# Optimization experiments

Measured on AMD Instinct MI355X. Metric: run time of the kernel, lower is better.

The kernel has to match this reference:

```python
import jax, jax.numpy as jnp
import numpy as np

E, H, B, S = 512, 8, 8, 1024  # embed_dim, n_head, batch, n_agent (sequence)
DH = E // H
DECAY_SCALING = 1.0


def _rmsnorm(x, scale, eps=1e-6):
    return x * jax.lax.rsqrt(jnp.mean(x * x, axis=-1, keepdims=True) + eps) * scale


def _groupnorm(y, scale, bias, n_head, eps=1e-5):
    # GroupNorm with num_groups = n_head over the feature axis (flax semantics).
    b, s, e = y.shape
    yg = y.reshape(b, s, n_head, e // n_head)
    mu = jnp.mean(yg, axis=-1, keepdims=True)
    var = jnp.var(yg, axis=-1, keepdims=True)
    yn = (yg - mu) * jax.lax.rsqrt(var + eps)
    return yn.reshape(b, s, e) * scale + bias


def _decay_kappas(n_head, scaling):
    # RetNet multi-scale decays: 1 - exp(linspace(log(1/32), log(1/512), H))
    k = 1.0 - jnp.exp(jnp.linspace(jnp.log(1.0 / 32.0), jnp.log(1.0 / 512.0), n_head))
    return (k * scaling).astype(jnp.float32)


def _msr(key_x, query_x, value_x, wq, wk, wv, wg, wo, gs, gb, kappas):
    # Parallel multi-scale retention (masked / causal, full_self_retention=False).
    b, s, e = query_x.shape
    h = wq.shape[0]
    q = jnp.einsum('bse,hed->bhsd', query_x, wq)
    k = jnp.einsum('bse,hed->bhsd', key_x, wk)
    v = jnp.einsum('bse,hed->bhsd', value_x, wv)
    n = jnp.arange(s)
    diff = n[:, None] - n[None, :]
    causal = diff >= 0
    expnt = jnp.where(causal, diff, 0).astype(q.dtype)
    # D[h,n,m] = kappa_h^(n-m) for n>=m else 0
    D = jnp.where(causal[None], kappas[:, None, None] ** expnt[None], 0.0)
    scores = jnp.einsum('bhnd,bhmd->bhnm', q, k) * D[None]  # [B,H,S,S]
    ret = jnp.einsum('bhnm,bhmd->bhnd', scores, v)
    ret = ret.transpose(0, 2, 1, 3).reshape(b, s, e)
    ret = _groupnorm(ret, gs, gb, h)
    return (jax.nn.swish(query_x @ wg) * ret) @ wo


def _swiglu(x, w_gate, w_lin, w_out):
    return (jax.nn.swish(x @ w_gate) * (x @ w_lin)) @ w_out


def setup_inputs() -> dict:
    key = jax.random.key(0)
    ks = jax.random.split(key, 20)
    sc = 0.02
    d = {
        'x': jax.random.normal(ks[0], (B, S, E), jnp.float32),
        'obs_rep': jax.random.normal(ks[1], (B, S, E), jnp.float32),
        # retention 1 params
        'wq1': jax.random.normal(ks[2], (H, E, DH), jnp.float32) * sc,
        'wk1': jax.random.normal(ks[3], (H, E, DH), jnp.float32) * sc,
        'wv1': jax.random.normal(ks[4], (H, E, DH), jnp.float32) * sc,
        'wg1': jax.random.normal(ks[5], (E, E), jnp.float32) * sc,
        'wo1': jax.random.normal(ks[6], (E, E), jnp.float32) * sc,
        'gs1': jnp.ones((E,), jnp.float32),
        'gb1': jnp.zeros((E,), jnp.float32),
        # retention 2 params
        'wq2': jax.random.normal(ks[7], (H, E, DH), jnp.float32) * sc,
        'wk2': jax.random.normal(ks[8], (H, E, DH), jnp.float32) * sc,
        'wv2': jax.random.normal(ks[9], (H, E, DH), jnp.float32) * sc,
        'wg2': jax.random.normal(ks[10], (E, E), jnp.float32) * sc,
        'wo2': jax.random.normal(ks[11], (E, E), jnp.float32) * sc,
        'gs2': jnp.ones((E,), jnp.float32),
        'gb2': jnp.zeros((E,), jnp.float32),
        # RMSNorm scales
        'ln1_s': jnp.ones((E,), jnp.float32),
        'ln2_s': jnp.ones((E,), jnp.float32),
        'ln3_s': jnp.ones((E,), jnp.float32),
        # SwiGLU(hidden=E, input=E)
        'ffn_w_lin': jax.random.normal(ks[12], (E, E), jnp.float32) * sc,
        'ffn_w_gate': jax.random.normal(ks[13], (E, E), jnp.float32) * sc,
        'ffn_w_out': jax.random.normal(ks[14], (E, E), jnp.float32) * sc,
    }
    return d


def reference(x, obs_rep, wq1, wk1, wv1, wg1, wo1, gs1, gb1,
              wq2, wk2, wv2, wg2, wo2, gs2, gb2,
              ln1_s, ln2_s, ln3_s, ffn_w_lin, ffn_w_gate, ffn_w_out):
    kappas = _decay_kappas(H, DECAY_SCALING)
    # x = ln1(x + retn1(key=x, query=x, value=x))
    x1 = _rmsnorm(x + _msr(x, x, x, wq1, wk1, wv1, wg1, wo1, gs1, gb1, kappas), ln1_s)
    # x = ln2(obs_rep + retn2(key=x1, query=obs_rep, value=x1))
    x2 = _rmsnorm(obs_rep + _msr(x1, obs_rep, x1, wq2, wk2, wv2, wg2, wo2, gs2, gb2, kappas), ln2_s)
    # out = ln3(x2 + ffn(x2))
    return _rmsnorm(x2 + _swiglu(x2, ffn_w_gate, ffn_w_lin, ffn_w_out), ln3_s)
```

## Files before the change

### kernel.cpp

```cpp
#include <hip/hip_runtime.h>
#include <hip/hip_bf16.h>
#include <stdint.h>

typedef unsigned short u16;
typedef unsigned int   u32;
typedef __bf16 bf16x8 __attribute__((ext_vector_type(8)));
typedef u16    u16x8  __attribute__((ext_vector_type(8)));
typedef float  f32x4  __attribute__((ext_vector_type(4)));

#define E_   512
#define H_   8
#define DH_  64
#define B_   8
#define S_   1024
#define M_   (B_ * S_)
#define NTOT (M_ * E_)

__device__ __forceinline__ u16 f2bf(float f) {
    u32 x = __float_as_uint(f);
    x += 0x7fffu + ((x >> 16) & 1u);
    return (u16)(x >> 16);
}
__device__ __forceinline__ float bf2f(u16 b) { return __uint_as_float((u32)b << 16); }
__device__ __forceinline__ bf16x8 as_bf(u16x8 v) {
    union { u16x8 u; bf16x8 b; } x; x.u = v; return x.b;
}
__device__ __forceinline__ u32 cvtpk(float lo, float hi) {
    u32 r;
    asm("v_cvt_pk_bf16_f32 %0, %1, %2" : "=v"(r) : "v"(lo), "v"(hi));
    return r;
}
__device__ __forceinline__ void gll16(const u16* g, u16* l) {
    __builtin_amdgcn_global_load_lds((const __attribute__((address_space(1))) u32*)g,
                                     (__attribute__((address_space(3))) u32*)l, 16, 0, 0);
}
__device__ __forceinline__ void xcd_map(int f, int nwg, int gx, int& bx, int& by) {
    int nf = (f & 7) * (nwg >> 3) + (f >> 3);
    bx = nf % gx; by = nf / gx;
}

__global__ __launch_bounds__(256) void prep_weights(
    const float* __restrict__ wq1, const float* __restrict__ wk1, const float* __restrict__ wv1,
    const float* __restrict__ wg1, const float* __restrict__ wq2, const float* __restrict__ wk2,
    const float* __restrict__ wv2, const float* __restrict__ wg2, const float* __restrict__ wgat,
    const float* __restrict__ wlin, const float* __restrict__ wo1, const float* __restrict__ wo2,
    const float* __restrict__ wout,
    u16* __restrict__ WC1, u16* __restrict__ WC2, u16* __restrict__ WF,
    u16* __restrict__ WO1t, u16* __restrict__ WO2t, u16* __restrict__ WOUt) {
    __shared__ float tle[64][65];
    const int rt = blockIdx.y, c0 = blockIdx.x * 64, tid = threadIdx.x;
    u16* dst; const float* src; int lr0; bool qkv = false; int nb0 = 0, h = 0;
    if (rt < 64) {
        bool s1 = rt < 32;
        dst = s1 ? WC1 : WC2;
        int r = (rt & 31) * 64; lr0 = r;
        if (r < 1536) {
            qkv = true; h = (r >> 6) & 7;
            src = (r < 512) ? (s1 ? wq1 : wq2) : (r < 1024) ? (s1 ? wk1 : wk2) : (s1 ? wv1 : wv2);
        } else { src = s1 ? wg1 : wg2; nb0 = r - 1536; }
    } else if (rt < 80) {
        dst = WF; int r = (rt - 64) * 64; lr0 = r;
        src = (r < 512) ? wgat : wlin; nb0 = r & 511;
    } else if (rt < 88) { dst = WO1t; lr0 = (rt - 80) * 64; src = wo1; nb0 = lr0; }
    else if (rt < 96)   { dst = WO2t; lr0 = (rt - 88) * 64; src = wo2; nb0 = lr0; }
    else                { dst = WOUt; lr0 = (rt - 96) * 64; src = wout; nb0 = lr0; }

    #pragma unroll
    for (int i = 0; i < 16; ++i) {
        int idx = i * 256 + tid, a = idx >> 6, b = idx & 63;
        tle[a][b] = qkv ? src[(size_t)(h * 512 + c0 + a) * 64 + b]
                        : src[(size_t)(c0 + a) * 512 + nb0 + b];
    }
    __syncthreads();
    #pragma unroll
    for (int i = 0; i < 16; ++i) {
        int idx = i * 256 + tid;
        dst[(size_t)(lr0 + (idx >> 6)) * 512 + c0 + (idx & 63)] = f2bf(tle[idx & 63][idx >> 6]);
    }
}

__global__ __launch_bounds__(256) void cvt_both(const float* __restrict__ x,
                                                const float* __restrict__ obs,
                                                u16* __restrict__ XB, u16* __restrict__ OB) {
    int i = blockIdx.x * 256 + threadIdx.x;
    float4 v = ((const float4*)x)[i];
    ushort4 o;
    o.x = f2bf(v.x); o.y = f2bf(v.y); o.z = f2bf(v.z); o.w = f2bf(v.w);
    ((ushort4*)XB)[i] = o;
    v = ((const float4*)obs)[i];
    o.x = f2bf(v.x); o.y = f2bf(v.y); o.z = f2bf(v.z); o.w = f2bf(v.w);
    ((ushort4*)OB)[i] = o;
}

__global__ __launch_bounds__(256) void gemm_qkvg(const u16* __restrict__ A1,
                                                 const u16* __restrict__ A2,
                                                 const u16* __restrict__ W,
                                                 u16* __restrict__ QB, u16* __restrict__ KB,
                                                 u16* __restrict__ KT, u16* __restrict__ VT,
                                                 u16* __restrict__ GB) {
    __shared__ u16 Als[128 * 64];
    __shared__ u16 Bls[128 * 64];
    const int tid = threadIdx.x;
    const int l = tid & 63, w = tid >> 6;
    const int wm = w & 1, wn = w >> 1;
    int bx, by; xcd_map(blockIdx.x, 1024, 16, bx, by);
    const int bm = by * 128, bn = bx * 128;
    const int which = bx >> 2;
    const u16* A = (which == 1 || which == 2) ? A2 : A1;

    size_t srcA[4], srcB[4]; int ldst[4];
    #pragma unroll
    for (int c = 0; c < 4; ++c) {
        int row = c * 32 + w * 8 + (l >> 3);
        int chs = (l & 7) ^ (row & 7);
        srcA[c] = (size_t)(bm + row) * E_ + chs * 8;
        srcB[c] = (size_t)(bn + row) * E_ + chs * 8;
        ldst[c] = c * 2048 + w * 512;
    }
    int aoff[2][4], boff[2][4];
    #pragma unroll
    for (int kk = 0; kk < 2; ++kk)
        #pragma unroll
        for (int f = 0; f < 4; ++f) {
            int ra = wm * 64 + f * 16 + (l & 15);
            int rb = wn * 64 + f * 16 + (l & 15);
            int ch = kk * 4 + (l >> 4);
            aoff[kk][f] = ra * 128 + ((ch ^ (ra & 7)) << 4);
            boff[kk][f] = rb * 128 + ((ch ^ (rb & 7)) << 4);
        }

    f32x4 acc[4][4] = {};
    for (int t = 0; t < 8; ++t) {
        const int k1 = t * 64;
        #pragma unroll
        for (int c = 0; c < 4; ++c) {
            gll16(A + srcA[c] + k1, &Als[ldst[c]]);
            gll16(W + srcB[c] + k1, &Bls[ldst[c]]);
        }
        __syncthreads();
        #pragma unroll
        for (int kk = 0; kk < 2; ++kk) {
            bf16x8 af[4], bfr[4];
            #pragma unroll
            for (int f = 0; f < 4; ++f) {
                af[f]  = as_bf(*(const u16x8*)((const char*)Als + aoff[kk][f]));
                bfr[f] = as_bf(*(const u16x8*)((const char*)Bls + boff[kk][f]));
            }
            #pragma unroll
            for (int m = 0; m < 4; ++m)
                #pragma unroll
                for (int n = 0; n < 4; ++n)
                    acc[m][n] = __builtin_amdgcn_mfma_f32_16x16x32_bf16(af[m], bfr[n], acc[m][n], 0, 0, 0);
        }
        __syncthreads();
    }

    #pragma unroll
    for (int m = 0; m < 4; ++m) {
        int row = bm + wm * 64 + m * 16 + ((l >> 4) << 2);
        #pragma unroll
        for (int n = 0; n < 4; ++n) {
            int coll = (bn & 511) + wn * 64 + n * 16 + (l & 15);
            f32x4 v = acc[m][n];
            size_t va = (((size_t)(row >> 10) * 8 + (coll >> 6)) * 64 + (coll & 63)) * 1024
                        + (row & 1023);
            if (which == 2) {
                ushort4 o;
                o.x = f2bf(v[0]); o.y = f2bf(v[1]); o.z = f2bf(v[2]); o.w = f2bf(v[3]);
                *(ushort4*)(VT + va) = o;
            } else if (which == 1) {
                #pragma unroll
                for (int r = 0; r < 4; ++r) KB[(size_t)(row + r) * E_ + coll] = f2bf(v[r]);
                ushort4 o;
                o.x = f2bf(v[0]); o.y = f2bf(v[1]); o.z = f2bf(v[2]); o.w = f2bf(v[3]);
                *(ushort4*)(KT + va) = o;
            } else {
                u16* dst = (which == 0) ? QB : GB;
                #pragma unroll
                for (int r = 0; r < 4; ++r) dst[(size_t)(row + r) * E_ + coll] = f2bf(v[r]);
            }
        }
    }
}

__global__ __launch_bounds__(256) void state_u(const u16* __restrict__ KT,
                                               const u16* __restrict__ VT,
                                               u16* __restrict__ U) {
    const int id = blockIdx.x;
    const int bh = id >> 3, c = id & 7;
    const int h = bh & 7;
    const int l = threadIdx.x & 63, w = threadIdx.x >> 6;
    const float kappa = 1.0f - __expf(-3.46573590f + (float)h * -0.39608410f);
    const float log2k = log2f(kappa);
    const float ik = 1.0f / kappa;

    bf16x8 af[4];
    {
        size_t vbase = ((size_t)bh * 64 + (w * 16 + (l & 15))) * 1024 + c * 128 + ((l >> 4) << 3);
        #pragma unroll
        for (int kk = 0; kk < 4; ++kk)
            af[kk] = as_bf(*(const u16x8*)(VT + vbase + kk * 32));
    }

    f32x4 acc[4] = {};
    #pragma unroll
    for (int fd = 0; fd < 4; ++fd) {
        size_t kbase = ((size_t)bh * 64 + (fd * 16 + (l & 15))) * 1024 + c * 128 + ((l >> 4) << 3);
        #pragma unroll
        for (int kk = 0; kk < 4; ++kk) {
            u16x8 kv = *(const u16x8*)(KT + kbase + kk * 32);
            int mb = kk * 32 + ((l >> 4) << 3);
            float wj = exp2f((float)(127 - mb) * log2k);
            u16x8 kw;
            #pragma unroll
            for (int j = 0; j < 8; ++j) { kw[j] = f2bf(bf2f(kv[j]) * wj); wj *= ik; }
            acc[fd] = __builtin_amdgcn_mfma_f32_16x16x32_bf16(af[kk], as_bf(kw), acc[fd], 0, 0, 0);
        }
    }

    #pragma unroll
    for (int fd = 0; fd < 4; ++fd) {
        int dv = w * 16 + ((l >> 4) << 2);
        int dk = fd * 16 + (l & 15);
        size_t ub = ((size_t)id * 64 + dv) * 64 + dk;
        #pragma unroll
        for (int r = 0; r < 4; ++r) U[ub + (size_t)r * 64] = f2bf(acc[fd][r]);
    }
}

__global__ __launch_bounds__(256) void retention_chunk(
        const u16* __restrict__ Q, const u16* __restrict__ K,
        const u16* __restrict__ VT, const u16* __restrict__ U,
        const u16* __restrict__ G,
        const float* __restrict__ gs, const float* __restrict__ gb,
        u16* __restrict__ T) {
    __shared__ u16 Ks[128 * 64], Vts[64 * 128], Ps[128 * 64], Ss[64 * 64];
    const int tid = threadIdx.x;
    const int l = tid & 63, w = tid >> 6;
    const int id = blockIdx.x;
    const int bh = id >> 3, c = id & 7;
    const int h = bh & 7;
    const int n0 = c * 128;
    const size_t base = (size_t)(bh >> 3) * (S_ * E_) + h * DH_;

    const float kappa = 1.0f - __expf(-3.46573590f + (float)h * -0.39608410f);
    const float log2k = log2f(kappa);
    const float ik = 1.0f / kappa;
    const float ikp2 = ik * ik, ikp3 = ikp2 * ik;

    float gsv[4], gbv[4];
    #pragma unroll
    for (int fd = 0; fd < 4; ++fd) {
        gsv[fd] = gs[h * 64 + fd * 16 + (l & 15)];
        gbv[fd] = gb[h * 64 + fd * 16 + (l & 15)];
    }

    #pragma unroll
    for (int cc = 0; cc < 4; ++cc) {
        int row = cc * 32 + w * 8 + (l >> 3);
        int chs = (l & 7) ^ (row & 7);
        gll16(K + base + (size_t)(n0 + row) * E_ + chs * 8, &Ks[cc * 2048 + w * 512]);
        int d = cc * 16 + w * 4 + (l >> 4);
        int vch = (l & 15) ^ (d & 15);
        gll16(VT + ((size_t)bh * 64 + d) * 1024 + n0 + vch * 8, &Vts[cc * 2048 + w * 512]);
    }

    bf16x8 qf[2][2];
    #pragma unroll
    for (int kk = 0; kk < 2; ++kk)
        #pragma unroll
        for (int fn = 0; fn < 2; ++fn) {
            int n = n0 + fn * 64 + w * 16 + (l & 15);
            qf[kk][fn] = as_bf(*(const u16x8*)(Q + base + (size_t)n * E_ + kk * 32 + ((l >> 4) << 3)));
        }

    if (c > 0) {
        float accs[16];
        #pragma unroll
        for (int j = 0; j < 16; ++j) accs[j] = 0.f;
        const float kC = exp2f(128.0f * log2k);
        float wc = 1.0f;
        size_t ub = (size_t)bh * (8 * 4096) + tid * 16;
        for (int cp = c - 1; cp >= 0; --cp) {
            const u16* up = U + ub + (size_t)cp * 4096;
            u16x8 a = *(const u16x8*)up;
            u16x8 b = *(const u16x8*)(up + 8);
            #pragma unroll
            for (int j = 0; j < 8; ++j) {
                accs[j]     += bf2f(a[j]) * wc;
                accs[8 + j] += bf2f(b[j]) * wc;
            }
            wc *= kC;
        }
        int dv = tid >> 2, ch0 = (tid & 3) << 1;
        #pragma unroll
        for (int hh = 0; hh < 2; ++hh) {
            uint4 pk;
            pk.x = cvtpk(accs[hh * 8 + 0], accs[hh * 8 + 1]);
            pk.y = cvtpk(accs[hh * 8 + 2], accs[hh * 8 + 3]);
            pk.z = cvtpk(accs[hh * 8 + 4], accs[hh * 8 + 5]);
            pk.w = cvtpk(accs[hh * 8 + 6], accs[hh * 8 + 7]);
            *(uint4*)((char*)Ss + dv * 128 + (((ch0 + hh) ^ (dv & 7)) << 4)) = pk;
        }
    }
    __syncthreads();

    f32x4 acc[2][4] = {};

    if (c > 0) {
        __builtin_amdgcn_s_setprio(1);
        #pragma unroll
        for (int kk = 0; kk < 2; ++kk) {
            bf16x8 sf[4];
            #pragma unroll
            for (int fd = 0; fd < 4; ++fd) {
                int dv = fd * 16 + (l & 15);
                int ch = kk * 4 + (l >> 4);
                sf[fd] = as_bf(*(const u16x8*)((const char*)Ss + dv * 128 + ((ch ^ (dv & 7)) << 4)));
            }
            #pragma unroll
            for (int fn = 0; fn < 2; ++fn)
                #pragma unroll
                for (int fd = 0; fd < 4; ++fd)
                    acc[fn][fd] = __builtin_amdgcn_mfma_f32_16x16x32_bf16(qf[kk][fn], sf[fd], acc[fn][fd], 0, 0, 0);
        }
        __builtin_amdgcn_s_setprio(0);
        #pragma unroll
        for (int fn = 0; fn < 2; ++fn) {
            int nl0 = fn * 64 + w * 16 + ((l >> 4) << 2);
            float fr0 = exp2f((float)(nl0 + 1) * log2k);
            float fr1 = fr0 * kappa, fr2 = fr1 * kappa, fr3 = fr2 * kappa;
            #pragma unroll
            for (int fd = 0; fd < 4; ++fd) {
                acc[fn][fd][0] *= fr0; acc[fn][fd][1] *= fr1;
                acc[fn][fd][2] *= fr2; acc[fn][fd][3] *= fr3;
            }
        }
    }

    #pragma unroll
    for (int mh = 0; mh < 2; ++mh) {
        const int m0l = mh * 64;
        bf16x8 kf[2][4];
        #pragma unroll
        for (int kk = 0; kk < 2; ++kk)
            #pragma unroll
            for (int f = 0; f < 4; ++f) {
                int row = m0l + f * 16 + (l & 15);
                int ch = kk * 4 + (l >> 4);
                kf[kk][f] = as_bf(*(const u16x8*)((const char*)Ks + row * 128 + ((ch ^ (row & 7)) << 4)));
            }
        #pragma unroll
        for (int fn = 0; fn < 2; ++fn) {
            if (mh == 1 && fn == 0) continue;
            f32x4 s[4] = {};
            __builtin_amdgcn_s_setprio(1);
            #pragma unroll
            for (int kk = 0; kk < 2; ++kk)
                #pragma unroll
                for (int f = 0; f < 4; ++f)
                    s[f] = __builtin_amdgcn_mfma_f32_16x16x32_bf16(kf[kk][f], qf[kk][fn], s[f], 0, 0, 0);
            __builtin_amdgcn_s_setprio(0);
            const bool fast = (mh == 0 && fn == 1);
            int nl = fn * 64 + w * 16 + (l & 15);
            #pragma unroll
            for (int f = 0; f < 4; ++f) {
                int mbl = m0l + f * 16 + ((l >> 4) << 2);
                int delta = nl - mbl;
                float wb = exp2f((float)delta * log2k);
                f32x4 v = s[f];
                float p0, p1, p2, p3;
                if (fast) {
                    float w1 = wb * ik, w2 = w1 * ik, w3 = w2 * ik;
                    p0 = v[0] * wb; p1 = v[1] * w1; p2 = v[2] * w2; p3 = v[3] * w3;
                } else {
                    p0 = (delta >= 0) ? v[0] * wb : 0.f;
                    p1 = (delta >= 1) ? v[1] * wb * ik : 0.f;
                    p2 = (delta >= 2) ? v[2] * wb * ikp2 : 0.f;
                    p3 = (delta >= 3) ? v[3] * wb * ikp3 : 0.f;
                }
                int mcl = f * 16 + ((l >> 4) << 2);
                int byteoff = nl * 128 + (((mcl >> 3) ^ (nl & 7)) << 4) + ((mcl & 4) << 1);
                uint2 pk;
                pk.x = cvtpk(p0, p1);
                pk.y = cvtpk(p2, p3);
                *(uint2*)((char*)Ps + byteoff) = pk;
            }
        }
        #pragma unroll
        for (int km = 0; km < 2; ++km) {
            bf16x8 pf[2];
            #pragma unroll
            for (int fn = 0; fn < 2; ++fn) {
                if (mh == 1 && fn == 0) continue;
                int row = fn * 64 + w * 16 + (l & 15);
                int ch = km * 4 + (l >> 4);
                pf[fn] = as_bf(*(const u16x8*)((const char*)Ps + row * 128 + ((ch ^ (row & 7)) << 4)));
            }
            __builtin_amdgcn_s_setprio(1);
            #pragma unroll
            for (int fd = 0; fd < 4; ++fd) {
                int d = fd * 16 + (l & 15);
                int mch = mh * 8 + km * 4 + (l >> 4);
                bf16x8 vfr = as_bf(*(const u16x8*)((const char*)Vts + d * 256 + ((mch ^ (d & 15)) << 4)));
                #pragma unroll
                for (int fn = 0; fn < 2; ++fn) {
                    if (mh == 1 && fn == 0) continue;
                    acc[fn][fd] = __builtin_amdgcn_mfma_f32_16x16x32_bf16(pf[fn], vfr, acc[fn][fd], 0, 0, 0);
                }
            }
            __builtin_amdgcn_s_setprio(0);
        }
    }

    #pragma unroll
    for (int fn = 0; fn < 2; ++fn) {
        #pragma unroll
        for (int r = 0; r < 4; ++r) {
            float s1 = 0.f, s2 = 0.f;
            #pragma unroll
            for (int fd = 0; fd < 4; ++fd) { float v = acc[fn][fd][r]; s1 += v; s2 += v * v; }
            #pragma unroll
            for (int off = 1; off < 16; off <<= 1) {
                s1 += __shfl_xor(s1, off, 64);
                s2 += __shfl_xor(s2, off, 64);
            }
            float mean = s1 * (1.f / 64.f);
            float var  = s2 * (1.f / 64.f) - mean * mean;
            float rinv = rsqrtf(var + 1e-5f);
            int rowg = n0 + fn * 64 + w * 16 + ((l >> 4) << 2) + r;
            size_t rb = base + (size_t)rowg * E_;
            #pragma unroll
            for (int fd = 0; fd < 4; ++fd) {
                int d = fd * 16 + (l & 15);
                float ny = (acc[fn][fd][r] - mean) * rinv;
                float rn = ny * gsv[fd] + gbv[fd];
                float g = bf2f(G[rb + d]);
                T[rb + d] = f2bf(g * rn / (1.f + __expf(-g)));
            }
        }
    }
}

__global__ __launch_bounds__(256) void gemm_wo(const u16* __restrict__ A,
                                               const u16* __restrict__ W,
                                               float* __restrict__ Cf) {
    __shared__ u16 Als[64 * 64];
    __shared__ u16 Bls[128 * 64];
    const int tid = threadIdx.x;
    const int l = tid & 63, w = tid >> 6;
    const int wm = w & 1, wn = w >> 1;
    int bx, by; xcd_map(blockIdx.x, 512, 4, bx, by);
    const int bm = by * 64, bn = bx * 128;

    size_t srcA[2], srcB[4]; int ldstA[2], ldstB[4];
    #pragma unroll
    for (int c = 0; c < 4; ++c) {
        int row = c * 32 + w * 8 + (l >> 3);
        int chs = (l & 7) ^ (row & 7);
        if (c < 2) { srcA[c] = (size_t)(bm + row) * E_ + chs * 8; ldstA[c] = c * 2048 + w * 512; }
        srcB[c] = (size_t)(bn + row) * E_ + chs * 8;
        ldstB[c] = c * 2048 + w * 512;
    }
    int aoff[2][2], boff[2][4];
    #pragma unroll
    for (int kk = 0; kk < 2; ++kk) {
        #pragma unroll
        for (int f = 0; f < 2; ++f) {
            int ra = wm * 32 + f * 16 + (l & 15);
            aoff[kk][f] = ra * 128 + (((kk * 4 + (l >> 4)) ^ (ra & 7)) << 4);
        }
        #pragma unroll
        for (int f = 0; f < 4; ++f) {
            int rb = wn * 64 + f * 16 + (l & 15);
            boff[kk][f] = rb * 128 + (((kk * 4 + (l >> 4)) ^ (rb & 7)) << 4);
        }
    }

    f32x4 acc[2][4] = {};
    for (int t = 0; t < 8; ++t) {
        const int k1 = t * 64;
        #pragma unroll
        for (int c = 0; c < 2; ++c) gll16(A + srcA[c] + k1, &Als[ldstA[c]]);
        #pragma unroll
        for (int c = 0; c < 4; ++c) gll16(W + srcB[c] + k1, &Bls[ldstB[c]]);
        __syncthreads();
        #pragma unroll
        for (int kk = 0; kk < 2; ++kk) {
            bf16x8 af[2], bfr[4];
            #pragma unroll
            for (int f = 0; f < 2; ++f) af[f] = as_bf(*(const u16x8*)((const char*)Als + aoff[kk][f]));
            #pragma unroll
            for (int f = 0; f < 4; ++f) bfr[f] = as_bf(*(const u16x8*)((const char*)Bls + boff[kk][f]));
            #pragma unroll
            for (int m = 0; m < 2; ++m)
                #pragma unroll
                for (int n = 0; n < 4; ++n)
                    acc[m][n] = __builtin_amdgcn_mfma_f32_16x16x32_bf16(af[m], bfr[n], acc[m][n], 0, 0, 0);
        }
        __syncthreads();
    }

    #pragma unroll
    for (int m = 0; m < 2; ++m) {
        int row = bm + wm * 32 + m * 16 + ((l >> 4) << 2);
        #pragma unroll
        for (int n = 0; n < 4; ++n) {
            int col = bn + wn * 64 + n * 16 + (l & 15);
            f32x4 v = acc[m][n];
            #pragma unroll
            for (int r = 0; r < 4; ++r) Cf[(size_t)(row + r) * E_ + col] = v[r];
        }
    }
}

__global__ __launch_bounds__(256) void gemm_ffn(const u16* __restrict__ A,
                                                const u16* __restrict__ W,
                                                u16* __restrict__ T) {
    __shared__ u16 Als[64 * 64];
    __shared__ u16 Bgs[64 * 64];
    __shared__ u16 Bls[64 * 64];
    const int tid = threadIdx.x;
    const int l = tid & 63, w = tid >> 6;
    const int wm = w & 1, wn = w >> 1;
    int bx, by; xcd_map(blockIdx.x, 1024, 8, bx, by);
    const int bm = by * 64, bn = bx * 64;

    size_t srcA[2], srcG[2], srcL[2]; int ldst[2];
    #pragma unroll
    for (int c = 0; c < 2; ++c) {
        int row = c * 32 + w * 8 + (l >> 3);
        int chs = (l & 7) ^ (row & 7);
        srcA[c] = (size_t)(bm + row) * E_ + chs * 8;
        srcG[c] = (size_t)(bn + row) * E_ + chs * 8;
        srcL[c] = (size_t)(512 + bn + row) * E_ + chs * 8;
        ldst[c] = c * 2048 + w * 512;
    }
    int aoff[2][2], goff[2][2];
    #pragma unroll
    for (int kk = 0; kk < 2; ++kk)
        #pragma unroll
        for (int f = 0; f < 2; ++f) {
            int ra = wm * 32 + f * 16 + (l & 15);
            int rb = wn * 32 + f * 16 + (l & 15);
            aoff[kk][f] = ra * 128 + (((kk * 4 + (l >> 4)) ^ (ra & 7)) << 4);
            goff[kk][f] = rb * 128 + (((kk * 4 + (l >> 4)) ^ (rb & 7)) << 4);
        }

    f32x4 accg[2][2] = {}, accl[2][2] = {};
    for (int t = 0; t < 8; ++t) {
        const int k1 = t * 64;
        #pragma unroll
        for (int c = 0; c < 2; ++c) {
            gll16(A + srcA[c] + k1, &Als[ldst[c]]);
            gll16(W + srcG[c] + k1, &Bgs[ldst[c]]);
            gll16(W + srcL[c] + k1, &Bls[ldst[c]]);
        }
        __syncthreads();
        #pragma unroll
        for (int kk = 0; kk < 2; ++kk) {
            bf16x8 af[2], bg[2], bl[2];
            #pragma unroll
            for (int f = 0; f < 2; ++f) {
                af[f] = as_bf(*(const u16x8*)((const char*)Als + aoff[kk][f]));
                bg[f] = as_bf(*(const u16x8*)((const char*)Bgs + goff[kk][f]));
                bl[f] = as_bf(*(const u16x8*)((const char*)Bls + goff[kk][f]));
            }
            #pragma unroll
            for (int m = 0; m < 2; ++m)
                #pragma unroll
                for (int n = 0; n < 2; ++n) {
                    accg[m][n] = __builtin_amdgcn_mfma_f32_16x16x32_bf16(af[m], bg[n], accg[m][n], 0, 0, 0);
                    accl[m][n] = __builtin_amdgcn_mfma_f32_16x16x32_bf16(af[m], bl[n], accl[m][n], 0, 0, 0);
                }
        }
        __syncthreads();
    }

    #pragma unroll
    for (int m = 0; m < 2; ++m) {
        int row = bm + wm * 32 + m * 16 + ((l >> 4) << 2);
        #pragma unroll
        for (int n = 0; n < 2; ++n) {
            int col = bn + wn * 32 + n * 16 + (l & 15);
            #pragma unroll
            for (int r = 0; r < 4; ++r) {
                float g = accg[m][n][r], lv = accl[m][n][r];
                T[(size_t)(row + r) * E_ + col] = f2bf(g * lv / (1.f + __expf(-g)));
            }
        }
    }
}

__global__ __launch_bounds__(512) void rmsnorm_res(const float* __restrict__ Xf,
                                                   const u16* __restrict__ Xb,
                                                   const float* __restrict__ Y,
                                                   const float* __restrict__ sc,
                                                   float* __restrict__ outf,
                                                   u16* __restrict__ outb) {
    __shared__ float part[8];
    size_t row = blockIdx.x;
    int t = threadIdx.x;
    float xv = Xf ? Xf[row * E_ + t] : bf2f(Xb[row * E_ + t]);
    float v = xv + Y[row * E_ + t];
    float sq = v * v;
    #pragma unroll
    for (int off = 1; off < 64; off <<= 1) sq += __shfl_xor(sq, off, 64);
    if ((t & 63) == 0) part[t >> 6] = sq;
    __syncthreads();
    float tot = 0.0f;
    #pragma unroll
    for (int i = 0; i < 8; ++i) tot += part[i];
    float r = rsqrtf(tot * (1.0f / 512.0f) + 1e-6f);
    float o = v * r * sc[t];
    if (outf) outf[row * E_ + t] = o;
    if (outb) outb[row * E_ + t] = f2bf(o);
}

extern "C" void kernel_launch(void* const* d_in, const int* in_sizes, int n_in,
                              void* d_out, int out_size, void* d_ws, size_t ws_size,
                              hipStream_t stream) {
    const float* x    = (const float*)d_in[0];
    const float* obs  = (const float*)d_in[1];
    const float* wq1  = (const float*)d_in[2];
    const float* wk1  = (const float*)d_in[3];
    const float* wv1  = (const float*)d_in[4];
    const float* wg1  = (const float*)d_in[5];
    const float* wo1  = (const float*)d_in[6];
    const float* gs1  = (const float*)d_in[7];
    const float* gb1  = (const float*)d_in[8];
    const float* wq2  = (const float*)d_in[9];
    const float* wk2  = (const float*)d_in[10];
    const float* wv2  = (const float*)d_in[11];
    const float* wg2  = (const float*)d_in[12];
    const float* wo2  = (const float*)d_in[13];
    const float* gs2  = (const float*)d_in[14];
    const float* gb2  = (const float*)d_in[15];
    const float* ln1s = (const float*)d_in[16];
    const float* ln2s = (const float*)d_in[17];
    const float* ln3s = (const float*)d_in[18];
    const float* wlin = (const float*)d_in[19];
    const float* wgat = (const float*)d_in[20];
    const float* wout = (const float*)d_in[21];

    u16* wsb = (u16*)d_ws;
    u16* WC1  = wsb;
    u16* WC2  = WC1 + 2048 * 512;
    u16* WF   = WC2 + 2048 * 512;
    u16* WO1t = WF + 1024 * 512;
    u16* WO2t = WO1t + 512 * 512;
    u16* WOUt = WO2t + 512 * 512;
    u16* XB   = WOUt + 512 * 512;
    u16* OB   = XB + NTOT;
    u16* QB   = OB + NTOT;
    u16* KB   = QB + NTOT;
    u16* KT   = KB + NTOT;
    u16* VT   = KT + NTOT;
    u16* GB   = VT + NTOT;
    u16* TB   = GB + NTOT;
    u16* UB   = TB + NTOT;
    float* GF = (float*)QB;

    dim3 tG(256);

    prep_weights<<<dim3(8, 104), tG, 0, stream>>>(wq1, wk1, wv1, wg1, wq2, wk2, wv2, wg2,
                                                  wgat, wlin, wo1, wo2, wout,
                                                  WC1, WC2, WF, WO1t, WO2t, WOUt);
    cvt_both<<<NTOT / 1024, tG, 0, stream>>>(x, obs, XB, OB);

    gemm_qkvg<<<1024, tG, 0, stream>>>(XB, XB, WC1, QB, KB, KT, VT, GB);
    state_u<<<512, tG, 0, stream>>>(KT, VT, UB);
    retention_chunk<<<512, tG, 0, stream>>>(QB, KB, VT, UB, GB, gs1, gb1, TB);
    gemm_wo<<<512, tG, 0, stream>>>(TB, WO1t, GF);
    rmsnorm_res<<<M_, 512, 0, stream>>>(x, nullptr, GF, ln1s, nullptr, XB);

    gemm_qkvg<<<1024, tG, 0, stream>>>(OB, XB, WC2, QB, KB, KT, VT, GB);
    state_u<<<512, tG, 0, stream>>>(KT, VT, UB);
    retention_chunk<<<512, tG, 0, stream>>>(QB, KB, VT, UB, GB, gs2, gb2, TB);
    gemm_wo<<<512, tG, 0, stream>>>(TB, WO2t, GF);
    rmsnorm_res<<<M_, 512, 0, stream>>>(obs, nullptr, GF, ln2s, nullptr, OB);

    gemm_ffn<<<1024, tG, 0, stream>>>(OB, WF, TB);
    gemm_wo<<<512, tG, 0, stream>>>(TB, WOUt, GF);
    rmsnorm_res<<<M_, 512, 0, stream>>>(nullptr, OB, GF, ln3s, (float*)d_out, nullptr);
}
```

Baseline: 203.6 us.

## Stage transposed K/V epilogue through LDS and enlarge FFN GEMM M-tile

The QKVG GEMM epilogue now writes the transposed K and V outputs by first packing bf16 pairs into a swizzled shared-memory tile. Each thread then emits contiguous 16-byte global stores, replacing scattered 8-byte strided writes. The FFN gate/lin GEMM tile grows from 64x64 to 128x64 rows per block, halving the grid and reusing weight tiles across more rows. This costs more shared memory and accumulator registers per block, plus an extra barrier in the epilogue.

```diff
diff --git a/kernel.cpp b/kernel.cpp
--- a/kernel.cpp
+++ b/kernel.cpp
@@ -98,8 +98,9 @@
                                                  u16* __restrict__ QB, u16* __restrict__ KB,
                                                  u16* __restrict__ KT, u16* __restrict__ VT,
                                                  u16* __restrict__ GB) {
-    __shared__ u16 Als[128 * 64];
-    __shared__ u16 Bls[128 * 64];
+    __shared__ u16 sh[16384];
+    u16* Als = sh;
+    u16* Bls = sh + 8192;
     const int tid = threadIdx.x;
     const int l = tid & 63, w = tid >> 6;
     const int wm = w & 1, wn = w >> 1;
@@ -155,30 +156,44 @@
         __syncthreads();
     }
 
-    #pragma unroll
-    for (int m = 0; m < 4; ++m) {
-        int row = bm + wm * 64 + m * 16 + ((l >> 4) << 2);
-        #pragma unroll
-        for (int n = 0; n < 4; ++n) {
-            int coll = (bn & 511) + wn * 64 + n * 16 + (l & 15);
-            f32x4 v = acc[m][n];
-            size_t va = (((size_t)(row >> 10) * 8 + (coll >> 6)) * 64 + (coll & 63)) * 1024
-                        + (row & 1023);
-            if (which == 2) {
-                ushort4 o;
-                o.x = f2bf(v[0]); o.y = f2bf(v[1]); o.z = f2bf(v[2]); o.w = f2bf(v[3]);
-                *(ushort4*)(VT + va) = o;
-            } else if (which == 1) {
-                #pragma unroll
-                for (int r = 0; r < 4; ++r) KB[(size_t)(row + r) * E_ + coll] = f2bf(v[r]);
-                ushort4 o;
-                o.x = f2bf(v[0]); o.y = f2bf(v[1]); o.z = f2bf(v[2]); o.w = f2bf(v[3]);
-                *(ushort4*)(KT + va) = o;
-            } else {
-                u16* dst = (which == 0) ? QB : GB;
+    if (which != 2) {
+        u16* dst = (which == 0) ? QB : (which == 1) ? KB : GB;
+        #pragma unroll
+        for (int m = 0; m < 4; ++m) {
+            int row = bm + wm * 64 + m * 16 + ((l >> 4) << 2);
+            #pragma unroll
+            for (int n = 0; n < 4; ++n) {
+                int coll = (bn & 511) + wn * 64 + n * 16 + (l & 15);
+                f32x4 v = acc[m][n];
                 #pragma unroll
                 for (int r = 0; r < 4; ++r) dst[(size_t)(row + r) * E_ + coll] = f2bf(v[r]);
             }
+        }
+    }
+    if (which == 1 || which == 2) {
+        u16* dstT = (which == 2) ? VT : KT;
+        #pragma unroll
+        for (int m = 0; m < 4; ++m) {
+            int row0 = wm * 64 + m * 16 + ((l >> 4) << 2);
+            #pragma unroll
+            for (int n = 0; n < 4; ++n) {
+                int c = wn * 64 + n * 16 + (l & 15);
+                f32x4 v = acc[m][n];
+                uint2 pk; pk.x = cvtpk(v[0], v[1]); pk.y = cvtpk(v[2], v[3]);
+                int off = c * 256 + (((row0 >> 3) ^ (c & 7)) << 4) + ((row0 & 7) << 1);
+                *(uint2*)((char*)sh + off) = pk;
+            }
+        }
+        __syncthreads();
+        int c = tid >> 1, half = tid & 1;
+        int collg = (bn & 511) + c;
+        int bh = ((bm >> 10) << 3) + (collg >> 6);
+        size_t gb = ((size_t)bh * 64 + (collg & 63)) * 1024 + (bm & 1023) + half * 64;
+        #pragma unroll
+        for (int j = 0; j < 8; ++j) {
+            int chunk = half * 8 + j;
+            uint4 vv = *(const uint4*)((const char*)sh + c * 256 + ((chunk ^ (c & 7)) << 4));
+            *(uint4*)(dstT + gb + j * 8) = vv;
         }
     }
 }
@@ -517,57 +532,66 @@
 __global__ __launch_bounds__(256) void gemm_ffn(const u16* __restrict__ A,
                                                 const u16* __restrict__ W,
                                                 u16* __restrict__ T) {
-    __shared__ u16 Als[64 * 64];
+    __shared__ u16 Als[128 * 64];
     __shared__ u16 Bgs[64 * 64];
-    __shared__ u16 Bls[64 * 64];
+    __shared__ u16 Bl2[64 * 64];
     const int tid = threadIdx.x;
     const int l = tid & 63, w = tid >> 6;
     const int wm = w & 1, wn = w >> 1;
-    int bx, by; xcd_map(blockIdx.x, 1024, 8, bx, by);
-    const int bm = by * 64, bn = bx * 64;
-
-    size_t srcA[2], srcG[2], srcL[2]; int ldst[2];
-    #pragma unroll
-    for (int c = 0; c < 2; ++c) {
+    int bx, by; xcd_map(blockIdx.x, 512, 8, bx, by);
+    const int bm = by * 128, bn = bx * 64;
+
+    size_t srcA[4], srcG[2], srcL[2]; int ldstA[4], ldstB[2];
+    #pragma unroll
+    for (int c = 0; c < 4; ++c) {
         int row = c * 32 + w * 8 + (l >> 3);
         int chs = (l & 7) ^ (row & 7);
         srcA[c] = (size_t)(bm + row) * E_ + chs * 8;
-        srcG[c] = (size_t)(bn + row) * E_ + chs * 8;
-        srcL[c] = (size_t)(512 + bn + row) * E_ + chs * 8;
-        ldst[c] = c * 2048 + w * 512;
-    }
-    int aoff[2][2], goff[2][2];
-    #pragma unroll
-    for (int kk = 0; kk < 2; ++kk)
+        ldstA[c] = c * 2048 + w * 512;
+        if (c < 2) {
+            srcG[c] = (size_t)(bn + row) * E_ + chs * 8;
+            srcL[c] = (size_t)(512 + bn + row) * E_ + chs * 8;
+            ldstB[c] = c * 2048 + w * 512;
+        }
+    }
+    int aoff[2][4], goff[2][2];
+    #pragma unroll
+    for (int kk = 0; kk < 2; ++kk) {
+        #pragma unroll
+        for (int f = 0; f < 4; ++f) {
+            int ra = wm * 64 + f * 16 + (l & 15);
+            aoff[kk][f] = ra * 128 + (((kk * 4 + (l >> 4)) ^ (ra & 7)) << 4);
+        }
         #pragma unroll
         for (int f = 0; f < 2; ++f) {
-            int ra = wm * 32 + f * 16 + (l & 15);
             int rb = wn * 32 + f * 16 + (l & 15);
-            aoff[kk][f] = ra * 128 + (((kk * 4 + (l >> 4)) ^ (ra & 7)) << 4);
             goff[kk][f] = rb * 128 + (((kk * 4 + (l >> 4)) ^ (rb & 7)) << 4);
         }
-
-    f32x4 accg[2][2] = {}, accl[2][2] = {};
+    }
+
+    f32x4 accg[4][2] = {}, accl[4][2] = {};
     for (int t = 0; t < 8; ++t) {
         const int k1 = t * 64;
         #pragma unroll
+        for (int c = 0; c < 4; ++c) gll16(A + srcA[c] + k1, &Als[ldstA[c]]);
+        #pragma unroll
         for (int c = 0; c < 2; ++c) {
-            gll16(A + srcA[c] + k1, &Als[ldst[c]]);
-            gll16(W + srcG[c] + k1, &Bgs[ldst[c]]);
-            gll16(W + srcL[c] + k1, &Bls[ldst[c]]);
+            gll16(W + srcG[c] + k1, &Bgs[ldstB[c]]);
+            gll16(W + srcL[c] + k1, &Bl2[ldstB[c]]);
         }
         __syncthreads();
         #pragma unroll
         for (int kk = 0; kk < 2; ++kk) {
-            bf16x8 af[2], bg[2], bl[2];
+            bf16x8 af[4], bg[2], bl[2];
+            #pragma unroll
+            for (int f = 0; f < 4; ++f) af[f] = as_bf(*(const u16x8*)((const char*)Als + aoff[kk][f]));
             #pragma unroll
             for (int f = 0; f < 2; ++f) {
-                af[f] = as_bf(*(const u16x8*)((const char*)Als + aoff[kk][f]));
                 bg[f] = as_bf(*(const u16x8*)((const char*)Bgs + goff[kk][f]));
-                bl[f] = as_bf(*(const u16x8*)((const char*)Bls + goff[kk][f]));
-            }
-            #pragma unroll
-            for (int m = 0; m < 2; ++m)
+                bl[f] = as_bf(*(const u16x8*)((const char*)Bl2 + goff[kk][f]));
+            }
+            #pragma unroll
+            for (int m = 0; m < 4; ++m)
                 #pragma unroll
                 for (int n = 0; n < 2; ++n) {
                     accg[m][n] = __builtin_amdgcn_mfma_f32_16x16x32_bf16(af[m], bg[n], accg[m][n], 0, 0, 0);
@@ -578,8 +602,8 @@
     }
 
     #pragma unroll
-    for (int m = 0; m < 2; ++m) {
-        int row = bm + wm * 32 + m * 16 + ((l >> 4) << 2);
+    for (int m = 0; m < 4; ++m) {
+        int row = bm + wm * 64 + m * 16 + ((l >> 4) << 2);
         #pragma unroll
         for (int n = 0; n < 2; ++n) {
             int col = bn + wn * 32 + n * 16 + (l & 15);
@@ -680,7 +704,7 @@
     gemm_wo<<<512, tG, 0, stream>>>(TB, WO2t, GF);
     rmsnorm_res<<<M_, 512, 0, stream>>>(obs, nullptr, GF, ln2s, nullptr, OB);
 
-    gemm_ffn<<<1024, tG, 0, stream>>>(OB, WF, TB);
+    gemm_ffn<<<512, tG, 0, stream>>>(OB, WF, TB);
     gemm_wo<<<512, tG, 0, stream>>>(TB, WOUt, GF);
     rmsnorm_res<<<M_, 512, 0, stream>>>(nullptr, OB, GF, ln3s, (float*)d_out, nullptr);
 }
```

After: 207.8 us. 2.0% more time.

## Transpose K/V epilogue through LDS and store projection outputs in bf16

Applied to the files above, without the earlier changes.

The QKVG GEMM epilogue now stages the K and V tiles in shared memory with an XOR swizzle, then writes the transposed KT/VT layout as coalesced 16-byte stores instead of scattered 8-byte column stores. Separately, the output-projection GEMMs write bf16 instead of fp32 and the RMSNorm-residual kernel reads bf16, which halves that intermediate's traffic. The bf16 intermediate adds rounding error before the residual add and norm, and the staging adds an extra barrier and LDS round trip in the epilogue.

```diff
diff --git a/kernel.cpp b/kernel.cpp
--- a/kernel.cpp
+++ b/kernel.cpp
@@ -98,8 +98,9 @@
                                                  u16* __restrict__ QB, u16* __restrict__ KB,
                                                  u16* __restrict__ KT, u16* __restrict__ VT,
                                                  u16* __restrict__ GB) {
-    __shared__ u16 Als[128 * 64];
-    __shared__ u16 Bls[128 * 64];
+    __shared__ u16 sh[16384];
+    u16* Als = sh;
+    u16* Bls = sh + 8192;
     const int tid = threadIdx.x;
     const int l = tid & 63, w = tid >> 6;
     const int wm = w & 1, wn = w >> 1;
@@ -155,30 +156,44 @@
         __syncthreads();
     }
 
-    #pragma unroll
-    for (int m = 0; m < 4; ++m) {
-        int row = bm + wm * 64 + m * 16 + ((l >> 4) << 2);
-        #pragma unroll
-        for (int n = 0; n < 4; ++n) {
-            int coll = (bn & 511) + wn * 64 + n * 16 + (l & 15);
-            f32x4 v = acc[m][n];
-            size_t va = (((size_t)(row >> 10) * 8 + (coll >> 6)) * 64 + (coll & 63)) * 1024
-                        + (row & 1023);
-            if (which == 2) {
-                ushort4 o;
-                o.x = f2bf(v[0]); o.y = f2bf(v[1]); o.z = f2bf(v[2]); o.w = f2bf(v[3]);
-                *(ushort4*)(VT + va) = o;
-            } else if (which == 1) {
-                #pragma unroll
-                for (int r = 0; r < 4; ++r) KB[(size_t)(row + r) * E_ + coll] = f2bf(v[r]);
-                ushort4 o;
-                o.x = f2bf(v[0]); o.y = f2bf(v[1]); o.z = f2bf(v[2]); o.w = f2bf(v[3]);
-                *(ushort4*)(KT + va) = o;
-            } else {
-                u16* dst = (which == 0) ? QB : GB;
+    if (which != 2) {
+        u16* dst = (which == 0) ? QB : (which == 1) ? KB : GB;
+        #pragma unroll
+        for (int m = 0; m < 4; ++m) {
+            int row = bm + wm * 64 + m * 16 + ((l >> 4) << 2);
+            #pragma unroll
+            for (int n = 0; n < 4; ++n) {
+                int coll = (bn & 511) + wn * 64 + n * 16 + (l & 15);
+                f32x4 v = acc[m][n];
                 #pragma unroll
                 for (int r = 0; r < 4; ++r) dst[(size_t)(row + r) * E_ + coll] = f2bf(v[r]);
             }
+        }
+    }
+    if (which == 1 || which == 2) {
+        u16* dstT = (which == 2) ? VT : KT;
+        #pragma unroll
+        for (int m = 0; m < 4; ++m) {
+            int row0 = wm * 64 + m * 16 + ((l >> 4) << 2);
+            #pragma unroll
+            for (int n = 0; n < 4; ++n) {
+                int c = wn * 64 + n * 16 + (l & 15);
+                f32x4 v = acc[m][n];
+                uint2 pk; pk.x = cvtpk(v[0], v[1]); pk.y = cvtpk(v[2], v[3]);
+                int off = c * 256 + (((row0 >> 3) ^ (c & 7)) << 4) + ((row0 & 7) << 1);
+                *(uint2*)((char*)sh + off) = pk;
+            }
+        }
+        __syncthreads();
+        int c = tid >> 1, half = tid & 1;
+        int collg = (bn & 511) + c;
+        int bh = ((bm >> 10) << 3) + (collg >> 6);
+        size_t gb = ((size_t)bh * 64 + (collg & 63)) * 1024 + (bm & 1023) + half * 64;
+        #pragma unroll
+        for (int j = 0; j < 8; ++j) {
+            int chunk = half * 8 + j;
+            uint4 vv = *(const uint4*)((const char*)sh + c * 256 + ((chunk ^ (c & 7)) << 4));
+            *(uint4*)(dstT + gb + j * 8) = vv;
         }
     }
 }
@@ -444,7 +459,7 @@
 
 __global__ __launch_bounds__(256) void gemm_wo(const u16* __restrict__ A,
                                                const u16* __restrict__ W,
-                                               float* __restrict__ Cf) {
+                                               u16* __restrict__ Cb) {
     __shared__ u16 Als[64 * 64];
     __shared__ u16 Bls[128 * 64];
     const int tid = threadIdx.x;
@@ -509,7 +524,7 @@
             int col = bn + wn * 64 + n * 16 + (l & 15);
             f32x4 v = acc[m][n];
             #pragma unroll
-            for (int r = 0; r < 4; ++r) Cf[(size_t)(row + r) * E_ + col] = v[r];
+            for (int r = 0; r < 4; ++r) Cb[(size_t)(row + r) * E_ + col] = f2bf(v[r]);
         }
     }
 }
@@ -594,7 +609,7 @@
 
 __global__ __launch_bounds__(512) void rmsnorm_res(const float* __restrict__ Xf,
                                                    const u16* __restrict__ Xb,
-                                                   const float* __restrict__ Y,
+                                                   const u16* __restrict__ Yb,
                                                    const float* __restrict__ sc,
                                                    float* __restrict__ outf,
                                                    u16* __restrict__ outb) {
@@ -602,7 +617,7 @@
     size_t row = blockIdx.x;
     int t = threadIdx.x;
     float xv = Xf ? Xf[row * E_ + t] : bf2f(Xb[row * E_ + t]);
-    float v = xv + Y[row * E_ + t];
+    float v = xv + bf2f(Yb[row * E_ + t]);
     float sq = v * v;
     #pragma unroll
     for (int off = 1; off < 64; off <<= 1) sq += __shfl_xor(sq, off, 64);
@@ -659,7 +674,7 @@
     u16* GB   = VT + NTOT;
     u16* TB   = GB + NTOT;
     u16* UB   = TB + NTOT;
-    float* GF = (float*)QB;
+    u16* YB   = QB;
 
     dim3 tG(256);
 
@@ -671,16 +686,16 @@
     gemm_qkvg<<<1024, tG, 0, stream>>>(XB, XB, WC1, QB, KB, KT, VT, GB);
     state_u<<<512, tG, 0, stream>>>(KT, VT, UB);
     retention_chunk<<<512, tG, 0, stream>>>(QB, KB, VT, UB, GB, gs1, gb1, TB);
-    gemm_wo<<<512, tG, 0, stream>>>(TB, WO1t, GF);
-    rmsnorm_res<<<M_, 512, 0, stream>>>(x, nullptr, GF, ln1s, nullptr, XB);
+    gemm_wo<<<512, tG, 0, stream>>>(TB, WO1t, YB);
+    rmsnorm_res<<<M_, 512, 0, stream>>>(x, nullptr, YB, ln1s, nullptr, XB);
 
     gemm_qkvg<<<1024, tG, 0, stream>>>(OB, XB, WC2, QB, KB, KT, VT, GB);
     state_u<<<512, tG, 0, stream>>>(KT, VT, UB);
     retention_chunk<<<512, tG, 0, stream>>>(QB, KB, VT, UB, GB, gs2, gb2, TB);
-    gemm_wo<<<512, tG, 0, stream>>>(TB, WO2t, GF);
-    rmsnorm_res<<<M_, 512, 0, stream>>>(obs, nullptr, GF, ln2s, nullptr, OB);
+    gemm_wo<<<512, tG, 0, stream>>>(TB, WO2t, YB);
+    rmsnorm_res<<<M_, 512, 0, stream>>>(obs, nullptr, YB, ln2s, nullptr, OB);
 
     gemm_ffn<<<1024, tG, 0, stream>>>(OB, WF, TB);
-    gemm_wo<<<512, tG, 0, stream>>>(TB, WOUt, GF);
-    rmsnorm_res<<<M_, 512, 0, stream>>>(nullptr, OB, GF, ln3s, (float*)d_out, nullptr);
-}
+    gemm_wo<<<512, tG, 0, stream>>>(TB, WOUt, YB);
+    rmsnorm_res<<<M_, 512, 0, stream>>>(nullptr, OB, YB, ln3s, (float*)d_out, nullptr);
+}
```

After: 204.4 us. Within noise of the previous version (+0.4%).
